# Optimization experiments

Measured on AMD Instinct MI355X. Metric: run time of the kernel, lower is better.

The kernel has to match this reference:

```python
import jax, jax.numpy as jnp
import numpy as np

B, C, N, M = 16, 256, 4096, 1024
EPS = 1e-5


def geometry_disentangle(x, num_select):
    # x: [B, C, N]. Variation score = L2 norm of mean-centered feature per point.
    score = jnp.linalg.norm(x - x.mean(axis=2, keepdims=True), axis=1)  # [B, N]
    _, idx_s = jax.lax.top_k(score, num_select)    # sharp: highest variation
    _, idx_g = jax.lax.top_k(-score, num_select)   # gentle: lowest variation
    sharp = jnp.take_along_axis(x, idx_s[:, None, :], axis=2)   # [B, C, M]
    gentle = jnp.take_along_axis(x, idx_g[:, None, :], axis=2)  # [B, C, M]
    return sharp, gentle


def cross_attention(x, ctx, Wq, bq, Wk, bk, Wv, bv, Wo, bo):
    # x: [B, C, N], ctx: [B, M, C] -> [B, C, N]
    c = x.shape[1]
    q = jnp.einsum('bcn,dc->bdn', x, Wq) + bq[None, :, None]  # conv1x1 on x
    k = jnp.einsum('bmc,dc->bmd', ctx, Wk) + bk
    v = jnp.einsum('bmc,dc->bmd', ctx, Wv) + bv
    scores = jnp.einsum('bdn,bmd->bnm', q, k) / jnp.sqrt(jnp.asarray(c, x.dtype))
    attn = jax.nn.softmax(scores, axis=-1)                     # [B, N, M]
    y = jnp.einsum('bnm,bmd->bdn', attn, v)                    # [B, C, N]
    y = jnp.einsum('bdn,ed->ben', y, Wo) + bo[None, :, None]   # output conv1x1
    return x + y


def conv_bn_relu(h, Wf, bf, gamma, beta):
    # Conv1d(k=1) + BatchNorm1d (training-mode batch stats) + ReLU. h: [B, 2C, N]
    y = jnp.einsum('bcn,dc->bdn', h, Wf) + bf[None, :, None]   # [B, C, N]
    mu = y.mean(axis=(0, 2), keepdims=True)
    var = y.var(axis=(0, 2), keepdims=True)
    y = (y - mu) * jax.lax.rsqrt(var + EPS)
    y = y * gamma[None, :, None] + beta[None, :, None]
    return jax.nn.relu(y)


def setup_inputs() -> dict:
    key = jax.random.key(0)
    ks = jax.random.split(key, 20)
    s = 0.02

    def w(k, shape):
        return (jax.random.normal(k, shape, dtype=jnp.float32) * s)

    inp = {
        'x': jax.random.normal(ks[0], (B, C, N), dtype=jnp.float32),
        'num_select': M,
        # sharp attention params
        'Wq_s': w(ks[1], (C, C)), 'bq_s': jnp.zeros((C,), jnp.float32),
        'Wk_s': w(ks[2], (C, C)), 'bk_s': jnp.zeros((C,), jnp.float32),
        'Wv_s': w(ks[3], (C, C)), 'bv_s': jnp.zeros((C,), jnp.float32),
        'Wo_s': w(ks[4], (C, C)), 'bo_s': jnp.zeros((C,), jnp.float32),
        # gentle attention params
        'Wq_g': w(ks[5], (C, C)), 'bq_g': jnp.zeros((C,), jnp.float32),
        'Wk_g': w(ks[6], (C, C)), 'bk_g': jnp.zeros((C,), jnp.float32),
        'Wv_g': w(ks[7], (C, C)), 'bv_g': jnp.zeros((C,), jnp.float32),
        'Wo_g': w(ks[8], (C, C)), 'bo_g': jnp.zeros((C,), jnp.float32),
        # fuse: Conv1d(2C -> C) + BN
        'Wf': w(ks[9], (C, 2 * C)), 'bf': jnp.zeros((C,), jnp.float32),
        'gamma': jnp.ones((C,), jnp.float32), 'beta': jnp.zeros((C,), jnp.float32),
    }
    return inp


def reference(x, Wq_s, bq_s, Wk_s, bk_s, Wv_s, bv_s, Wo_s, bo_s,
              Wq_g, bq_g, Wk_g, bk_g, Wv_g, bv_g, Wo_g, bo_g,
              Wf, bf, gamma, beta, num_select):
    sharp, gentle = geometry_disentangle(x, num_select)
    y_s = cross_attention(x, sharp.transpose(0, 2, 1), Wq_s, bq_s, Wk_s, bk_s, Wv_s, bv_s, Wo_s, bo_s)
    y_g = cross_attention(x, gentle.transpose(0, 2, 1), Wq_g, bq_g, Wk_g, bk_g, Wv_g, bv_g, Wo_g, bo_g)
    h = jnp.concatenate([y_s, y_g], axis=1)  # [B, 2C, N]
    return conv_bn_relu(h, Wf, bf, gamma, beta)
```

## Files before the change

### kernel.cpp

```cpp
#include <hip/hip_runtime.h>

#define BB 16
#define CC 256
#define NN 4096
#define MM 1024
#define EPSV 1e-5f
#define SCALE (1.0f/16.0f)

#define OFF_MU    0
#define OFF_SCORE 4096
#define OFF_IDX   69632
#define OFF_U     102400
#define OFF_WVZ   167936
#define OFF_WF12  233472
#define OFF_BVZ   299008
#define OFF_BZ    299264
#define OFF_W16   299520
#define OFF_XG    430592
#define OFF_K16   2527744
#define OFF_VT16  4624896
#define OFF_Z     6722048
#define OFF_BN    23499264
#define FIXED_F   23499776

typedef __attribute__((ext_vector_type(8))) short s16x8;
typedef __attribute__((ext_vector_type(4))) float f32x4;

__device__ __forceinline__ unsigned short f2bf(float f) {
    unsigned int u = __float_as_uint(f);
    return (unsigned short)((u + 0x7FFFu + ((u >> 16) & 1u)) >> 16);
}
__device__ __forceinline__ float bf2f(unsigned short h) {
    return __uint_as_float(((unsigned int)h) << 16);
}

__global__ __launch_bounds__(256) void zero_bn_kernel(float* bn) {
    int t = threadIdx.x;
    bn[t] = 0.f; bn[t + CC] = 0.f;
}

__global__ __launch_bounds__(256) void zero_rsum_kernel(float* r) {
    r[blockIdx.x * 256 + threadIdx.x] = 0.f;
}

__global__ __launch_bounds__(256) void mean_kernel(const float* __restrict__ x, float* __restrict__ mu) {
    int c = blockIdx.x, b = blockIdx.y, t = threadIdx.x;
    const float4* p = (const float4*)(x + ((size_t)b * CC + c) * NN);
    float s = 0.f;
    for (int n = t; n < NN / 4; n += 256) { float4 v = p[n]; s += (v.x + v.y) + (v.z + v.w); }
    __shared__ float red[256];
    red[t] = s; __syncthreads();
    for (int w = 128; w > 0; w >>= 1) { if (t < w) red[t] += red[t + w]; __syncthreads(); }
    if (t == 0) mu[b * CC + c] = red[0] * (1.0f / NN);
}

__global__ __launch_bounds__(256) void transpose_score_kernel(const float* __restrict__ x,
                                                              const float* __restrict__ mu,
                                                              unsigned short* __restrict__ xT,
                                                              float* __restrict__ score) {
    __shared__ float tile[32][33];
    __shared__ float smu[32];
    int b = blockIdx.z, c0 = blockIdx.y * 32, n0 = blockIdx.x * 32, t = threadIdx.x;
    int nl = t & 31, cr = t >> 5;
    if (t < 32) smu[t] = mu[b * CC + c0 + t];
#pragma unroll
    for (int q = 0; q < 4; ++q)
        tile[cr + q * 8][nl] = x[((size_t)b * CC + c0 + cr + q * 8) * NN + n0 + nl];
    __syncthreads();
    int nr = t >> 3, cq = t & 7;
    uint2 p;
    p.x = (unsigned int)f2bf(tile[cq * 4 + 0][nr]) | ((unsigned int)f2bf(tile[cq * 4 + 1][nr]) << 16);
    p.y = (unsigned int)f2bf(tile[cq * 4 + 2][nr]) | ((unsigned int)f2bf(tile[cq * 4 + 3][nr]) << 16);
    *(uint2*)&xT[((size_t)b * NN + n0 + nr) * CC + c0 + cq * 4] = p;
    int n = t & 31, cseg = t >> 5;
    float part = 0.f;
#pragma unroll
    for (int q = 0; q < 4; ++q) {
        float d = tile[cseg * 4 + q][n] - smu[cseg * 4 + q];
        part += d * d;
    }
    __syncthreads();
    tile[n][cseg] = part;
    __syncthreads();
    if (t < 32) {
        float s = 0.f;
#pragma unroll
        for (int j = 0; j < 8; ++j) s += tile[t][j];
        atomicAdd(&score[(size_t)b * NN + n0 + t], s);
    }
}

__global__ __launch_bounds__(1024) void select_kernel(const float* __restrict__ score,
                                                      int* __restrict__ idx_s, int* __restrict__ idx_g) {
    int b = blockIdx.x, t = threadIdx.x;
    __shared__ unsigned int keys[NN];
    __shared__ unsigned int hist[256];
    __shared__ unsigned int sbin, skrem;
    __shared__ int outcnt, eqcnt;
    __shared__ int eqidx[NN];
    for (int q = t; q < NN; q += 1024) keys[q] = __float_as_uint(score[(size_t)b * NN + q]);
    __syncthreads();
    for (int r = 0; r < 2; ++r) {
        unsigned int flip = r ? 0xFFFFFFFFu : 0u;
        unsigned int prefix = 0u, pmask = 0u;
        unsigned int k = MM;
        for (int pass = 0; pass < 4; ++pass) {
            int shift = 24 - 8 * pass;
            if (t < 256) hist[t] = 0u;
            __syncthreads();
            for (int q = t; q < NN; q += 1024) {
                unsigned int kv = keys[q] ^ flip;
                if ((kv & pmask) == prefix) atomicAdd(&hist[(kv >> shift) & 255u], 1u);
            }
            __syncthreads();
            for (int off = 1; off < 256; off <<= 1) {
                unsigned int v = 0u;
                if (t < 256) v = hist[t] + ((t + off < 256) ? hist[t + off] : 0u);
                __syncthreads();
                if (t < 256) hist[t] = v;
                __syncthreads();
            }
            if (t < 256) {
                unsigned int sj = hist[t], sj1 = (t < 255) ? hist[t + 1] : 0u;
                if (sj >= k && sj1 < k) { sbin = (unsigned int)t; skrem = k - sj1; }
            }
            __syncthreads();
            prefix |= sbin << shift;
            pmask |= 0xFFu << shift;
            k = skrem;
            __syncthreads();
        }
        unsigned int T = prefix;
        unsigned int krem = k;
        int* outp = r ? idx_g : idx_s;
        if (t == 0) { outcnt = 0; eqcnt = 0; }
        __syncthreads();
        for (int q = t; q < NN; q += 1024) {
            unsigned int kv = keys[q] ^ flip;
            if (kv > T) { int pp = atomicAdd(&outcnt, 1); outp[(size_t)b * MM + pp] = q; }
            else if (kv == T) { int pp = atomicAdd(&eqcnt, 1); eqidx[pp] = q; }
        }
        __syncthreads();
        int ne = eqcnt;
        for (int i = t; i < ne; i += 1024) {
            int me = eqidx[i];
            int rank = 0;
            for (int j = 0; j < ne; ++j) rank += (eqidx[j] < me) ? 1 : 0;
            if (rank < (int)krem) { int pp = atomicAdd(&outcnt, 1); outp[(size_t)b * MM + pp] = me; }
        }
        __syncthreads();
    }
}

__global__ __launch_bounds__(256) void smallmm_kernel(const float* __restrict__ A, int lda, int aoff,
                                                      const float* __restrict__ Bm, float* __restrict__ Cm) {
    int e = blockIdx.x, t = threadIdx.x;
    __shared__ float arow[CC];
    arow[t] = A[e * lda + aoff + t];
    __syncthreads();
    float acc = 0.f;
    for (int k = 0; k < CC; ++k) acc += arow[k] * Bm[k * CC + t];
    Cm[e * CC + t] = acc;
}

__global__ __launch_bounds__(256) void bvz_kernel(const float* __restrict__ U, const float* __restrict__ bv,
                                                  float* __restrict__ bvz) {
    int e = threadIdx.x;
    float acc = 0.f;
    for (int d = 0; d < CC; ++d) acc += U[e * CC + d] * bv[d];
    bvz[e] = acc;
}

__global__ __launch_bounds__(256) void bz_kernel(const float* __restrict__ Wf, const float* __restrict__ bf,
                                                 const float* __restrict__ bo_s, const float* __restrict__ bo_g,
                                                 float* __restrict__ bz) {
    int e = threadIdx.x;
    float acc = bf[e];
    for (int c = 0; c < CC; ++c)
        acc += Wf[e * 2 * CC + c] * bo_s[c] + Wf[e * 2 * CC + CC + c] * bo_g[c];
    bz[e] = acc;
}

__global__ __launch_bounds__(256) void wf12_kernel(const float* __restrict__ Wf, float* __restrict__ Wf12) {
    int e = blockIdx.x, c = threadIdx.x;
    Wf12[e * CC + c] = Wf[e * 2 * CC + c] + Wf[e * 2 * CC + CC + c];
}

__global__ __launch_bounds__(256) void conv_bf16_kernel(const float* __restrict__ src,
                                                        unsigned short* __restrict__ dst) {
    int i = blockIdx.x * 256 + threadIdx.x;
    float4 v = *(const float4*)(src + (size_t)i * 4);
    uint2 p;
    p.x = (unsigned int)f2bf(v.x) | ((unsigned int)f2bf(v.y) << 16);
    p.y = (unsigned int)f2bf(v.z) | ((unsigned int)f2bf(v.w) << 16);
    *(uint2*)&dst[(size_t)i * 4] = p;
}

__global__ __launch_bounds__(256) void gather_kernel(const unsigned short* __restrict__ xT,
                                                     const int* __restrict__ idx,
                                                     unsigned short* __restrict__ Xg) {
    int row = blockIdx.x * 4 + (threadIdx.x >> 6);
    int l = threadIdx.x & 63;
    int b = row >> 10, m = row & (MM - 1);
    int src = idx[b * MM + m];
    *(uint2*)&Xg[(size_t)row * CC + l * 4] =
        *(const uint2*)&xT[((size_t)b * NN + src) * CC + l * 4];
}

template<int OMODE>
__global__ __launch_bounds__(256, 3) void gemm_bt(
    const unsigned short* __restrict__ A, size_t a_bs,
    const unsigned short* __restrict__ Bw, size_t b_bs,
    const float* __restrict__ bias,
    void* __restrict__ outp, size_t o_bs, int ldo)
{
    __shared__ __align__(16) unsigned short As[128 * 32];
    __shared__ __align__(16) unsigned short Bs[128 * 32];
    int z = blockIdx.z;
    const unsigned short* Ab = A + z * a_bs + (size_t)blockIdx.x * 128 * CC;
    const unsigned short* Bb = Bw + z * b_bs + (size_t)blockIdx.y * 128 * CC;
    int t = threadIdx.x, w = t >> 6, l = t & 63, g = l >> 4, c16 = l & 15;
    int wi = w >> 1, wj = w & 1;
    int srow = t >> 2, skq = (t & 3) * 8;

    f32x4 acc[4][4];
#pragma unroll
    for (int a = 0; a < 4; ++a)
#pragma unroll
        for (int bq = 0; bq < 4; ++bq) acc[a][bq] = (f32x4){0.f, 0.f, 0.f, 0.f};

    for (int ks = 0; ks < 8; ++ks) {
        int k0 = ks * 32;
        uint4 a0 = *(const uint4*)(Ab + (size_t)srow * CC + k0 + skq);
        uint4 a1 = *(const uint4*)(Ab + (size_t)(srow + 64) * CC + k0 + skq);
        uint4 b0 = *(const uint4*)(Bb + (size_t)srow * CC + k0 + skq);
        uint4 b1 = *(const uint4*)(Bb + (size_t)(srow + 64) * CC + k0 + skq);
        __syncthreads();
        *(uint4*)&As[srow * 32 + skq] = a0;
        *(uint4*)&As[(srow + 64) * 32 + skq] = a1;
        *(uint4*)&Bs[srow * 32 + skq] = b0;
        *(uint4*)&Bs[(srow + 64) * 32 + skq] = b1;
        __syncthreads();
        s16x8 af[4], bf4[4];
#pragma unroll
        for (int fi = 0; fi < 4; ++fi)
            af[fi] = *(const s16x8*)&As[(wi * 64 + fi * 16 + c16) * 32 + g * 8];
#pragma unroll
        for (int fj = 0; fj < 4; ++fj)
            bf4[fj] = *(const s16x8*)&Bs[(wj * 64 + fj * 16 + c16) * 32 + g * 8];
#pragma unroll
        for (int fi = 0; fi < 4; ++fi)
#pragma unroll
            for (int fj = 0; fj < 4; ++fj)
                acc[fi][fj] = __builtin_amdgcn_mfma_f32_16x16x32_bf16(af[fi], bf4[fj], acc[fi][fj], 0, 0, 0);
    }

    int i0 = blockIdx.x * 128 + wi * 64, j0 = blockIdx.y * 128 + wj * 64;
#pragma unroll
    for (int fi = 0; fi < 4; ++fi) {
#pragma unroll
        for (int fj = 0; fj < 4; ++fj) {
            int colg = j0 + fj * 16 + c16;
#pragma unroll
            for (int r = 0; r < 4; ++r) {
                int rowg = i0 + fi * 16 + g * 4 + r;
                float v = acc[fi][fj][r] + (OMODE == 2 ? bias[rowg] : bias[colg]);
                if (OMODE == 0)
                    ((float*)outp)[z * o_bs + (size_t)rowg * ldo + colg] = v;
                else
                    ((unsigned short*)outp)[z * o_bs + (size_t)rowg * ldo + colg] = f2bf(v);
            }
        }
    }
}

__global__ __attribute__((amdgpu_flat_work_group_size(512, 512)))
__attribute__((amdgpu_waves_per_eu(2, 2)))
void fused_attn(
    const unsigned short* __restrict__ Q,
    const unsigned short* __restrict__ K,
    const unsigned short* __restrict__ Vt,
    float* __restrict__ Z)
{
    extern __shared__ __align__(16) unsigned char smem[];
    float* rsl = (float*)(smem + 114688);

    int z = blockIdx.z;
    int n0 = blockIdx.x * 128;
    int t = threadIdx.x, w = t >> 6, l = t & 63, g = l >> 4, c16 = l & 15;
    int wn = w >> 1, wc = w & 1;

    const unsigned short* Qb = Q + ((size_t)z * NN + n0) * CC;
    const char* Kzb = (const char*)(K + (size_t)z * MM * CC);
    const char* Vzb = (const char*)(Vt + (size_t)z * CC * MM);

    s16x8 q[2][8];
#pragma unroll
    for (int fi = 0; fi < 2; ++fi)
#pragma unroll
        for (int ks = 0; ks < 8; ++ks)
            q[fi][ks] = *(const s16x8*)&Qb[(size_t)(wn * 32 + fi * 16 + c16) * CC + ks * 32 + g * 8];

    f32x4 o[2][8];
#pragma unroll
    for (int fi = 0; fi < 2; ++fi)
#pragma unroll
        for (int fj = 0; fj < 8; ++fj) o[fi][fj] = (f32x4){0.f, 0.f, 0.f, 0.f};
    float rs[2][4];
#pragma unroll
    for (int fi = 0; fi < 2; ++fi)
#pragma unroll
        for (int r = 0; r < 4; ++r) rs[fi][r] = 0.f;

    auto issueK = [&](int buf, int m0) {
#pragma unroll
        for (int j = 0; j < 2; ++j) {
            int cid = w * 2 + j;
            int row = cid * 2 + (l >> 5);
            int srcoff = ((l & 31) * 16) ^ ((row & 7) << 4);
            const char* gp = Kzb + (size_t)(m0 + row) * 512 + srcoff;
            __builtin_amdgcn_global_load_lds(
                (const __attribute__((address_space(1))) void*)gp,
                (__attribute__((address_space(3))) void*)(smem + buf * 16384 + cid * 1024),
                16, 0, 0);
        }
    };
    auto issueV = [&](int slot, int m0) {
#pragma unroll
        for (int j = 0; j < 2; ++j) {
            int cid = w * 2 + j;
            int row = cid * 16 + (l >> 2);
            int srcoff = ((l & 3) * 16) ^ ((row & 3) << 4);
            const char* gp = Vzb + (size_t)row * 2048 + (size_t)m0 * 2 + srcoff;
            __builtin_amdgcn_global_load_lds(
                (const __attribute__((address_space(1))) void*)gp,
                (__attribute__((address_space(3))) void*)(smem + 32768 + slot * 16384 + cid * 1024),
                16, 0, 0);
        }
    };

    auto qk_exp = [&](int buf, int par) {
        const unsigned char* Ks = smem + buf * 16384;
        unsigned char* Ps = smem + 81920 + par * 16384;
        f32x4 sacc[2];
#pragma unroll
        for (int fi = 0; fi < 2; ++fi) sacc[fi] = (f32x4){0.f, 0.f, 0.f, 0.f};
        int mr = wc * 16 + c16;
        __builtin_amdgcn_s_setprio(1);
#pragma unroll
        for (int ks = 0; ks < 8; ++ks) {
            s16x8 kf = *(const s16x8*)(Ks + ((mr * 512 + ks * 64 + g * 16) ^ ((mr & 7) << 4)));
#pragma unroll
            for (int fi = 0; fi < 2; ++fi)
                sacc[fi] = __builtin_amdgcn_mfma_f32_16x16x32_bf16(q[fi][ks], kf, sacc[fi], 0, 0, 0);
        }
        __builtin_amdgcn_s_setprio(0);
        int mc = wc * 16 + c16;
#pragma unroll
        for (int fi = 0; fi < 2; ++fi)
#pragma unroll
            for (int r = 0; r < 4; ++r) {
                float e = __expf(sacc[fi][r] * SCALE);
                unsigned short h = f2bf(e);
                int nr = wn * 32 + fi * 16 + g * 4 + r;
                *(unsigned short*)(Ps + ((nr * 128 + mc * 2) ^ ((nr & 7) << 4))) = h;
                rs[fi][r] += bf2f(h);
            }
    };
    auto pv = [&](int slot, int par) {
        const unsigned char* Vs = smem + 32768 + slot * 16384;
        const unsigned char* Ps = smem + 81920 + par * 16384;
        s16x8 pa[2];
#pragma unroll
        for (int fi = 0; fi < 2; ++fi) {
            int nr = wn * 32 + fi * 16 + c16;
            pa[fi] = *(const s16x8*)(Ps + ((nr * 128 + g * 16) ^ ((nr & 7) << 4)));
        }
        __builtin_amdgcn_s_setprio(1);
#pragma unroll
        for (int fj = 0; fj < 8; ++fj) {
            int er = wc * 128 + fj * 16 + c16;
            s16x8 vb = *(const s16x8*)(Vs + ((er * 64 + g * 16) ^ ((er & 3) << 4)));
#pragma unroll
            for (int fi = 0; fi < 2; ++fi)
                o[fi][fj] = __builtin_amdgcn_mfma_f32_16x16x32_bf16(pa[fi], vb, o[fi][fj], 0, 0, 0);
        }
        __builtin_amdgcn_s_setprio(0);
    };

    issueK(0, 0); issueV(0, 0);
    issueK(1, 32); issueV(1, 32);
    __syncthreads();
    qk_exp(0, 0);

    for (int mt = 0; mt < 32; ++mt) {
        __syncthreads();
        if (mt < 30) {
            issueK(mt & 1, (mt + 2) * 32);
            issueV((mt + 2) % 3, (mt + 2) * 32);
        }
        __builtin_amdgcn_sched_barrier(0);
        if (mt < 31) qk_exp((mt + 1) & 1, (mt + 1) & 1);
        pv(mt % 3, mt & 1);
    }

#pragma unroll
    for (int fi = 0; fi < 2; ++fi)
#pragma unroll
        for (int r = 0; r < 4; ++r) {
            float v = rs[fi][r];
            v += __shfl_xor(v, 1); v += __shfl_xor(v, 2);
            v += __shfl_xor(v, 4); v += __shfl_xor(v, 8);
            if (c16 == 0) rsl[wc * 128 + wn * 32 + fi * 16 + g * 4 + r] = v;
        }
    __syncthreads();
    float* Zb = Z + ((size_t)z * NN + n0) * CC;
#pragma unroll
    for (int fi = 0; fi < 2; ++fi)
#pragma unroll
        for (int r = 0; r < 4; ++r) {
            int nr = wn * 32 + fi * 16 + g * 4 + r;
            float inv = 1.0f / (rsl[nr] + rsl[128 + nr]);
#pragma unroll
            for (int fj = 0; fj < 8; ++fj) {
                int e = wc * 128 + fj * 16 + c16;
                Zb[(size_t)nr * CC + e] += o[fi][fj][r] * inv;
            }
        }
}

__global__ __launch_bounds__(256) void bn_stats_kernel(const float* __restrict__ Z, float* __restrict__ bn) {
    int blk = blockIdx.x, e = threadIdx.x;
    const float* p = Z + (size_t)blk * 256 * CC + e;
    float s1 = 0.f, s2 = 0.f;
    for (int r = 0; r < 256; ++r) { float v = p[(size_t)r * CC]; s1 += v; s2 += v * v; }
    atomicAdd(&bn[e], s1);
    atomicAdd(&bn[CC + e], s2);
}

__global__ __launch_bounds__(256) void bn_apply_kernel(const float* __restrict__ Z, const float* __restrict__ bn,
                                                       const float* __restrict__ gamma, const float* __restrict__ beta,
                                                       float* __restrict__ out) {
    int b = blockIdx.z, e0 = blockIdx.y * 32, n0 = blockIdx.x * 32, t = threadIdx.x;
    __shared__ float tile[32][33];
    int c = t & 31, r0 = (t >> 5) * 4;
#pragma unroll
    for (int q = 0; q < 4; ++q)
        tile[r0 + q][c] = Z[((size_t)b * NN + n0 + r0 + q) * CC + e0 + c];
    __syncthreads();
    int n = t & 31, er0 = (t >> 5) * 4;
    const float invcnt = 1.0f / (BB * NN);
#pragma unroll
    for (int q = 0; q < 4; ++q) {
        int e = e0 + er0 + q;
        float mean = bn[e] * invcnt;
        float var = bn[CC + e] * invcnt - mean * mean;
        float rsq = rsqrtf(var + EPSV);
        float v = (tile[n][er0 + q] - mean) * rsq * gamma[e] + beta[e];
        out[((size_t)b * CC + e) * NN + n0 + n] = fmaxf(v, 0.f);
    }
}

extern "C" void kernel_launch(void* const* d_in, const int* in_sizes, int n_in,
                              void* d_out, int out_size, void* d_ws, size_t ws_size,
                              hipStream_t stream) {
    const float* x    = (const float*)d_in[0];
    const float* Wq_s = (const float*)d_in[2];  const float* bq_s = (const float*)d_in[3];
    const float* Wk_s = (const float*)d_in[4];  const float* bk_s = (const float*)d_in[5];
    const float* Wv_s = (const float*)d_in[6];  const float* bv_s = (const float*)d_in[7];
    const float* Wo_s = (const float*)d_in[8];  const float* bo_s = (const float*)d_in[9];
    const float* Wq_g = (const float*)d_in[10]; const float* bq_g = (const float*)d_in[11];
    const float* Wk_g = (const float*)d_in[12]; const float* bk_g = (const float*)d_in[13];
    const float* Wv_g = (const float*)d_in[14]; const float* bv_g = (const float*)d_in[15];
    const float* Wo_g = (const float*)d_in[16]; const float* bo_g = (const float*)d_in[17];
    const float* Wf   = (const float*)d_in[18]; const float* bf   = (const float*)d_in[19];
    const float* gamma = (const float*)d_in[20]; const float* beta = (const float*)d_in[21];

    float* ws    = (float*)d_ws;
    float* mu    = ws + OFF_MU;
    float* score = ws + OFF_SCORE;
    int*   idx_s = (int*)(ws + OFF_IDX);
    int*   idx_g = idx_s + BB * MM;
    float* U     = ws + OFF_U;
    float* Wvz   = ws + OFF_WVZ;
    float* Wf12  = ws + OFF_WF12;
    float* bvz   = ws + OFF_BVZ;
    float* bz    = ws + OFF_BZ;
    unsigned short* Wf12_16 = (unsigned short*)(ws + OFF_W16);
    unsigned short* Wq16    = Wf12_16 + 65536;
    unsigned short* Wk16    = Wq16 + 65536;
    unsigned short* Wvz16   = Wk16 + 65536;
    unsigned short* Xg16 = (unsigned short*)(ws + OFF_XG);
    unsigned short* K16  = (unsigned short*)(ws + OFF_K16);
    unsigned short* Vt16 = (unsigned short*)(ws + OFF_VT16);
    float* Z     = ws + OFF_Z;
    float* bn    = ws + OFF_BN;
    unsigned short* Q16  = (unsigned short*)d_out;
    unsigned short* xT16 = Q16 + (size_t)BB * NN * CC;

    zero_bn_kernel<<<1, 256, 0, stream>>>(bn);
    mean_kernel<<<dim3(CC, BB), 256, 0, stream>>>(x, mu);
    zero_rsum_kernel<<<BB * NN / 256, 256, 0, stream>>>(score);
    transpose_score_kernel<<<dim3(NN / 32, CC / 32, BB), 256, 0, stream>>>(x, mu, xT16, score);
    select_kernel<<<BB, 1024, 0, stream>>>(score, idx_s, idx_g);
    wf12_kernel<<<CC, 256, 0, stream>>>(Wf, Wf12);
    bz_kernel<<<1, 256, 0, stream>>>(Wf, bf, bo_s, bo_g, bz);
    conv_bf16_kernel<<<64, 256, 0, stream>>>(Wf12, Wf12_16);
    gemm_bt<0><<<dim3(512, 2, 1), 256, 0, stream>>>(xT16, 0, Wf12_16, 0, bz, Z, 0, CC);

    for (int br = 0; br < 2; ++br) {
        const float* Wo = br ? Wo_g : Wo_s;
        const float* Wv = br ? Wv_g : Wv_s;  const float* bv = br ? bv_g : bv_s;
        const float* Wk = br ? Wk_g : Wk_s;  const float* bk = br ? bk_g : bk_s;
        const float* Wq = br ? Wq_g : Wq_s;  const float* bq = br ? bq_g : bq_s;
        int* idx = br ? idx_g : idx_s;
        int aoff = br ? CC : 0;
        smallmm_kernel<<<CC, 256, 0, stream>>>(Wf, 2 * CC, aoff, Wo, U);
        smallmm_kernel<<<CC, 256, 0, stream>>>(U, CC, 0, Wv, Wvz);
        bvz_kernel<<<1, 256, 0, stream>>>(U, bv, bvz);
        conv_bf16_kernel<<<64, 256, 0, stream>>>(Wq, Wq16);
        conv_bf16_kernel<<<64, 256, 0, stream>>>(Wk, Wk16);
        conv_bf16_kernel<<<64, 256, 0, stream>>>(Wvz, Wvz16);
        gather_kernel<<<BB * MM / 4, 256, 0, stream>>>(xT16, idx, Xg16);
        gemm_bt<1><<<dim3(BB * MM / 128, 2, 1), 256, 0, stream>>>(Xg16, 0, Wk16, 0, bk, K16, 0, CC);
        gemm_bt<2><<<dim3(2, 8, BB), 256, 0, stream>>>(Wvz16, 0, Xg16, (size_t)MM * CC, bvz,
                                                       Vt16, (size_t)CC * MM, MM);
        gemm_bt<1><<<dim3(512, 2, 1), 256, 0, stream>>>(xT16, 0, Wq16, 0, bq, Q16, 0, CC);

        fused_attn<<<dim3(NN / 128, 1, BB), 512, 115712, stream>>>(Q16, K16, Vt16, Z);
    }

    bn_stats_kernel<<<BB * NN / 256, 256, 0, stream>>>(Z, bn);
    bn_apply_kernel<<<dim3(NN / 32, CC / 32, BB), 256, 0, stream>>>(Z, bn, gamma, beta, (float*)d_out);
}
```

Baseline: 630.7 us.

## Fold Wq into key projection to skip Q GEMM, add per-key bias term

Rewrites q·k as x^T (Wq^T Wk) xg plus bias terms: a combined W2 = Wq^T Wk is precomputed and applied on the gathered keys, so the attention kernel reads x (bf16 transposed) directly as Q and the large per-branch Q projection GEMM over all N points is removed. A per-key scalar beta (from bq) is computed separately and added before exp. This removes a B*N*C*C GEMM and its Q write per branch, at the cost of a small extra kernels and slight precision change from bf16 W2. It also changes the V tile LDS swizzle pattern to reduce bank conflicts.

```diff
diff --git a/kernel.cpp b/kernel.cpp
--- a/kernel.cpp
+++ b/kernel.cpp
@@ -186,6 +186,41 @@
     Wf12[e * CC + c] = Wf[e * 2 * CC + c] + Wf[e * 2 * CC + CC + c];
 }
 
+__global__ __launch_bounds__(256) void w2_kernel(const float* __restrict__ Wq, const float* __restrict__ Wk,
+                                                 float* __restrict__ W2) {
+    int d = blockIdx.x, t = threadIdx.x;
+    __shared__ float aq[CC];
+    aq[t] = Wq[t * CC + d];
+    __syncthreads();
+    float acc = 0.f;
+    for (int c = 0; c < CC; ++c) acc += aq[c] * Wk[c * CC + t];
+    W2[d * CC + t] = acc;
+}
+
+__global__ __launch_bounds__(256) void ub2_kernel(const float* __restrict__ Wq, const float* __restrict__ Wk,
+                                                  const float* __restrict__ bq, const float* __restrict__ bk,
+                                                  float* __restrict__ u, float* __restrict__ b2) {
+    int t = threadIdx.x;
+    float au = 0.f, ab = 0.f;
+    for (int c = 0; c < CC; ++c) { au += bq[c] * Wk[c * CC + t]; ab += Wq[c * CC + t] * bk[c]; }
+    u[t] = au; b2[t] = ab;
+    if (t == 0) { float s = 0.f; for (int c = 0; c < CC; ++c) s += bq[c] * bk[c]; u[CC] = s; }
+}
+
+__global__ __launch_bounds__(256) void beta_kernel(const unsigned short* __restrict__ Xg,
+                                                   const float* __restrict__ u, float* __restrict__ beta) {
+    int row = blockIdx.x * 4 + (threadIdx.x >> 6);
+    int l = threadIdx.x & 63;
+    uint2 p = *(const uint2*)&Xg[(size_t)row * CC + l * 4];
+    float acc = bf2f((unsigned short)(p.x & 0xFFFF)) * u[l * 4]
+              + bf2f((unsigned short)(p.x >> 16)) * u[l * 4 + 1]
+              + bf2f((unsigned short)(p.y & 0xFFFF)) * u[l * 4 + 2]
+              + bf2f((unsigned short)(p.y >> 16)) * u[l * 4 + 3];
+    acc += __shfl_xor(acc, 1); acc += __shfl_xor(acc, 2); acc += __shfl_xor(acc, 4);
+    acc += __shfl_xor(acc, 8); acc += __shfl_xor(acc, 16); acc += __shfl_xor(acc, 32);
+    if (l == 0) beta[row] = acc + u[CC];
+}
+
 __global__ __launch_bounds__(256) void conv_bf16_kernel(const float* __restrict__ src,
                                                         unsigned short* __restrict__ dst) {
     int i = blockIdx.x * 256 + threadIdx.x;
@@ -280,10 +315,12 @@
     const unsigned short* __restrict__ Q,
     const unsigned short* __restrict__ K,
     const unsigned short* __restrict__ Vt,
+    const float* __restrict__ beta,
     float* __restrict__ Z)
 {
     extern __shared__ __align__(16) unsigned char smem[];
     float* rsl = (float*)(smem + 114688);
+    float* bs  = (float*)(smem + 115712);
 
     int z = blockIdx.z;
     int n0 = blockIdx.x * 128;
@@ -293,6 +330,9 @@
     const unsigned short* Qb = Q + ((size_t)z * NN + n0) * CC;
     const char* Kzb = (const char*)(K + (size_t)z * MM * CC);
     const char* Vzb = (const char*)(Vt + (size_t)z * CC * MM);
+
+    bs[t] = beta[(size_t)z * MM + t];
+    bs[t + 512] = beta[(size_t)z * MM + t + 512];
 
     s16x8 q[2][8];
 #pragma unroll
@@ -330,7 +370,7 @@
         for (int j = 0; j < 2; ++j) {
             int cid = w * 2 + j;
             int row = cid * 16 + (l >> 2);
-            int srcoff = ((l & 3) * 16) ^ ((row & 3) << 4);
+            int srcoff = ((l & 3) * 16) ^ (((row >> 1) & 3) << 4);
             const char* gp = Vzb + (size_t)row * 2048 + (size_t)m0 * 2 + srcoff;
             __builtin_amdgcn_global_load_lds(
                 (const __attribute__((address_space(1))) void*)gp,
@@ -339,7 +379,7 @@
         }
     };
 
-    auto qk_exp = [&](int buf, int par) {
+    auto qk_exp = [&](int buf, int par, int m0) {
         const unsigned char* Ks = smem + buf * 16384;
         unsigned char* Ps = smem + 81920 + par * 16384;
         f32x4 sacc[2];
@@ -355,15 +395,15 @@
                 sacc[fi] = __builtin_amdgcn_mfma_f32_16x16x32_bf16(q[fi][ks], kf, sacc[fi], 0, 0, 0);
         }
         __builtin_amdgcn_s_setprio(0);
-        int mc = wc * 16 + c16;
+        float bet = bs[m0 + wc * 16 + c16];
 #pragma unroll
         for (int fi = 0; fi < 2; ++fi)
 #pragma unroll
             for (int r = 0; r < 4; ++r) {
-                float e = __expf(sacc[fi][r] * SCALE);
+                float e = __expf((sacc[fi][r] + bet) * SCALE);
                 unsigned short h = f2bf(e);
                 int nr = wn * 32 + fi * 16 + g * 4 + r;
-                *(unsigned short*)(Ps + ((nr * 128 + mc * 2) ^ ((nr & 7) << 4))) = h;
+                *(unsigned short*)(Ps + ((nr * 128 + (wc * 16 + c16) * 2) ^ ((nr & 7) << 4))) = h;
                 rs[fi][r] += bf2f(h);
             }
     };
@@ -380,7 +420,7 @@
 #pragma unroll
         for (int fj = 0; fj < 8; ++fj) {
             int er = wc * 128 + fj * 16 + c16;
-            s16x8 vb = *(const s16x8*)(Vs + ((er * 64 + g * 16) ^ ((er & 3) << 4)));
+            s16x8 vb = *(const s16x8*)(Vs + ((er * 64 + g * 16) ^ (((er >> 1) & 3) << 4)));
 #pragma unroll
             for (int fi = 0; fi < 2; ++fi)
                 o[fi][fj] = __builtin_amdgcn_mfma_f32_16x16x32_bf16(pa[fi], vb, o[fi][fj], 0, 0, 0);
@@ -391,7 +431,7 @@
     issueK(0, 0); issueV(0, 0);
     issueK(1, 32); issueV(1, 32);
     __syncthreads();
-    qk_exp(0, 0);
+    qk_exp(0, 0, 0);
 
     for (int mt = 0; mt < 32; ++mt) {
         __syncthreads();
@@ -400,7 +440,7 @@
             issueV((mt + 2) % 3, (mt + 2) * 32);
         }
         __builtin_amdgcn_sched_barrier(0);
-        if (mt < 31) qk_exp((mt + 1) & 1, (mt + 1) & 1);
+        if (mt < 31) qk_exp((mt + 1) & 1, (mt + 1) & 1, (mt + 1) * 32);
         pv(mt % 3, mt & 1);
     }
 
@@ -486,17 +526,19 @@
     float* Wf12  = ws + OFF_WF12;
     float* bvz   = ws + OFF_BVZ;
     float* bz    = ws + OFF_BZ;
+    float* W2    = ws + OFF_WF12;
+    float* uvec  = ws + OFF_MU;
+    float* b2    = ws + OFF_MU + 512;
+    float* betaA = ws + OFF_SCORE;
     unsigned short* Wf12_16 = (unsigned short*)(ws + OFF_W16);
-    unsigned short* Wq16    = Wf12_16 + 65536;
-    unsigned short* Wk16    = Wq16 + 65536;
-    unsigned short* Wvz16   = Wk16 + 65536;
+    unsigned short* W2_16   = Wf12_16 + 65536;
+    unsigned short* Wvz16   = W2_16 + 65536;
     unsigned short* Xg16 = (unsigned short*)(ws + OFF_XG);
     unsigned short* K16  = (unsigned short*)(ws + OFF_K16);
     unsigned short* Vt16 = (unsigned short*)(ws + OFF_VT16);
     float* Z     = ws + OFF_Z;
     float* bn    = ws + OFF_BN;
-    unsigned short* Q16  = (unsigned short*)d_out;
-    unsigned short* xT16 = Q16 + (size_t)BB * NN * CC;
+    unsigned short* xT16 = (unsigned short*)d_out + (size_t)BB * NN * CC;
 
     zero_bn_kernel<<<1, 256, 0, stream>>>(bn);
     mean_kernel<<<dim3(CC, BB), 256, 0, stream>>>(x, mu);
@@ -518,16 +560,17 @@
         smallmm_kernel<<<CC, 256, 0, stream>>>(Wf, 2 * CC, aoff, Wo, U);
         smallmm_kernel<<<CC, 256, 0, stream>>>(U, CC, 0, Wv, Wvz);
         bvz_kernel<<<1, 256, 0, stream>>>(U, bv, bvz);
-        conv_bf16_kernel<<<64, 256, 0, stream>>>(Wq, Wq16);
-        conv_bf16_kernel<<<64, 256, 0, stream>>>(Wk, Wk16);
+        w2_kernel<<<CC, 256, 0, stream>>>(Wq, Wk, W2);
+        ub2_kernel<<<1, 256, 0, stream>>>(Wq, Wk, bq, bk, uvec, b2);
+        conv_bf16_kernel<<<64, 256, 0, stream>>>(W2, W2_16);
         conv_bf16_kernel<<<64, 256, 0, stream>>>(Wvz, Wvz16);
         gather_kernel<<<BB * MM / 4, 256, 0, stream>>>(xT16, idx, Xg16);
-        gemm_bt<1><<<dim3(BB * MM / 128, 2, 1), 256, 0, stream>>>(Xg16, 0, Wk16, 0, bk, K16, 0, CC);
+        gemm_bt<1><<<dim3(BB * MM / 128, 2, 1), 256, 0, stream>>>(Xg16, 0, W2_16, 0, b2, K16, 0, CC);
+        beta_kernel<<<BB * MM / 4, 256, 0, stream>>>(Xg16, uvec, betaA);
         gemm_bt<2><<<dim3(2, 8, BB), 256, 0, stream>>>(Wvz16, 0, Xg16, (size_t)MM * CC, bvz,
                                                        Vt16, (size_t)CC * MM, MM);
-        gemm_bt<1><<<dim3(512, 2, 1), 256, 0, stream>>>(xT16, 0, Wq16, 0, bq, Q16, 0, CC);
-
-        fused_attn<<<dim3(NN / 128, 1, BB), 512, 115712, stream>>>(Q16, K16, Vt16, Z);
+
+        fused_attn<<<dim3(NN / 128, 1, BB), 512, 119808, stream>>>(xT16, K16, Vt16, betaA, Z);
     }
 
     bn_stats_kernel<<<BB * NN / 256, 256, 0, stream>>>(Z, bn);
```

Measured after the change: 649.4 us. +3.0%, slower.
